# Kernel optimization log

Hardware: AMD Instinct MI355X
Metric: run time of the kernel (lower is better)

## Reference

```python
import jax, jax.numpy as jnp
import numpy as np

D_MODEL = 1024
NUM_HEADS = 16
HEAD_DIM = D_MODEL // NUM_HEADS


def setup_inputs() -> dict:
    key = jax.random.key(0)
    ks = jax.random.split(key, 11)
    B, S = 2, 2048
    sc = 1.0 / np.sqrt(D_MODEL)
    inp = {
        "query": jax.random.normal(ks[0], (B, S, D_MODEL), jnp.float32),
        "key": jax.random.normal(ks[1], (B, S, D_MODEL), jnp.float32),
        "value": jax.random.normal(ks[2], (B, S, D_MODEL), jnp.float32),
        "Wq": jax.random.normal(ks[3], (D_MODEL, D_MODEL), jnp.float32) * sc,
        "bq": jnp.zeros((D_MODEL,), jnp.float32),
        "Wk": jax.random.normal(ks[4], (D_MODEL, D_MODEL), jnp.float32) * sc,
        "bk": jnp.zeros((D_MODEL,), jnp.float32),
        "Wv": jax.random.normal(ks[5], (D_MODEL, D_MODEL), jnp.float32) * sc,
        "bv": jnp.zeros((D_MODEL,), jnp.float32),
        "Wo": jax.random.normal(ks[6], (D_MODEL, D_MODEL), jnp.float32) * sc,
        "bo": jnp.zeros((D_MODEL,), jnp.float32),
    }
    return inp


def _split_heads(x):
    B, S, _ = x.shape
    return x.reshape(B, S, NUM_HEADS, HEAD_DIM).transpose(0, 2, 1, 3)  # [B,H,S,Dh]


def reference(query, key, value, Wq, bq, Wk, bk, Wv, bv, Wo, bo):
    Q = _split_heads(query @ Wq.T + bq)
    K = _split_heads(key @ Wk.T + bk)
    V = _split_heads(value @ Wv.T + bv)
    scores = jnp.einsum("bhqd,bhkd->bhqk", Q, K) / jnp.sqrt(jnp.float32(HEAD_DIM))
    attn = jax.nn.softmax(scores, axis=-1)  # dropout = identity (eval)
    out = jnp.einsum("bhqk,bhkd->bhqd", attn, V)
    B, H, S, Dh = out.shape
    out = out.transpose(0, 2, 1, 3).reshape(B, S, H * Dh)
    return out @ Wo.T + bo
```

## Files before the change

### kernel.cpp

```cpp
#include <hip/hip_runtime.h>
#include <hip/hip_bf16.h>

typedef __attribute__((ext_vector_type(8))) short short8;
typedef __attribute__((ext_vector_type(4))) short short4v;
typedef __attribute__((ext_vector_type(4))) float f32x4;
typedef __attribute__((ext_vector_type(16))) float f32x16;
typedef __attribute__((ext_vector_type(4))) int int4v;
typedef __attribute__((ext_vector_type(2))) int int2v;

#define DEV static __device__ __forceinline__

constexpr int S_LEN   = 2048;
constexpr int DMODEL  = 1024;
constexpr int NHEAD   = 16;
constexpr int DHEAD   = 64;
constexpr int NBATCH  = 2;
constexpr int BHN     = NBATCH * NHEAD;
constexpr int MROWS   = NBATCH * S_LEN;
constexpr int NDIM    = DMODEL;

DEV unsigned short f2b(float f) {
  __hip_bfloat16 h = __float2bfloat16(f);
  return __builtin_bit_cast(unsigned short, h);
}
DEV unsigned pk2(float a, float b) {
  return (unsigned)f2b(a) | ((unsigned)f2b(b) << 16);
}
DEV short8 ld8(const void* p) {
  return *reinterpret_cast<const short8*>(p);
}
DEV f32x4 mfma16(short8 a, short8 b, f32x4 c) {
  return __builtin_amdgcn_mfma_f32_16x16x32_bf16(a, b, c, 0, 0, 0);
}
DEV f32x16 mfma32(short8 a, short8 b, f32x16 c) {
  return __builtin_amdgcn_mfma_f32_32x32x16_bf16(a, b, c, 0, 0, 0);
}
DEV void gload16(const void* g, void* l) {
  __builtin_amdgcn_global_load_lds(
      (const __attribute__((address_space(1))) unsigned*)g,
      (__attribute__((address_space(3))) unsigned*)l, 16, 0, 0);
}

struct CvtArgs {
  const float* src[7];
  unsigned short* dst[7];
  int n4[7];
};

__global__ __launch_bounds__(256) void cvt_bf16(CvtArgs c) {
  const int seg = blockIdx.y;
  const float* __restrict__ s = c.src[seg];
  unsigned short* __restrict__ d = c.dst[seg];
  const int n4 = c.n4[seg];
  for (int i = blockIdx.x * 256 + threadIdx.x; i < n4; i += gridDim.x * 256) {
    f32x4 v = reinterpret_cast<const f32x4*>(s)[i];
    short4v r;
    r[0] = (short)f2b(v[0]); r[1] = (short)f2b(v[1]);
    r[2] = (short)f2b(v[2]); r[3] = (short)f2b(v[3]);
    reinterpret_cast<short4v*>(d)[i] = r;
  }
}

struct GB {
  const unsigned short* A[3];
  const unsigned short* W[3];
  const float* bia[3];
  void* out[3];
  int epi[3];
};

__global__ __launch_bounds__(256, 2) void gemm_bf16(GB g) {
  const int z = blockIdx.z;
  const unsigned short* __restrict__ A = g.A[z];
  const unsigned short* __restrict__ W = g.W[z];
  const float* __restrict__ bia = g.bia[z];
  const int epi = g.epi[z];
  const int bm = blockIdx.y, bn = blockIdx.x;
  const int tid = threadIdx.x, lane = tid & 63, wid = tid >> 6;
  const int wr = wid >> 1, wc = wid & 1;
  const int fr = lane & 15, gq = lane >> 4;

  __shared__ unsigned short As[2][128][32];
  __shared__ unsigned short Bs[2][128][32];

  f32x4 acc[4][4] = {};

  const int srow = lane >> 2;
  const int scol = (lane & 3) * 16;
  const char* aS = (const char*)A + (size_t)(bm * 128 + wid * 16 + srow) * 2048 + scol;
  const char* bS = (const char*)W + (size_t)(bn * 128 + wid * 16 + srow) * 2048 + scol;

  auto stage = [&](int buf, int kt) {
    const int ko = kt * 64;
    char* a0 = (char*)As[buf] + wid * 1024;
    char* b0 = (char*)Bs[buf] + wid * 1024;
    gload16(aS + ko, a0);
    gload16(aS + (size_t)64 * 2048 + ko, a0 + 4096);
    gload16(bS + ko, b0);
    gload16(bS + (size_t)64 * 2048 + ko, b0 + 4096);
  };

  stage(0, 0);
  __syncthreads();
  for (int kt = 0; kt < 32; ++kt) {
    const int buf = kt & 1;
    if (kt + 1 < 32) stage(buf ^ 1, kt + 1);
    short8 af[4], bf4[4];
#pragma unroll
    for (int i = 0; i < 4; ++i) af[i] = ld8(&As[buf][wr * 64 + i * 16 + fr][gq * 8]);
#pragma unroll
    for (int j = 0; j < 4; ++j) bf4[j] = ld8(&Bs[buf][wc * 64 + j * 16 + fr][gq * 8]);
#pragma unroll
    for (int i = 0; i < 4; ++i)
#pragma unroll
      for (int j = 0; j < 4; ++j)
        acc[i][j] = mfma16(af[i], bf4[j], acc[i][j]);
    __syncthreads();
  }

#pragma unroll
  for (int i = 0; i < 4; ++i) {
#pragma unroll
    for (int j = 0; j < 4; ++j) {
#pragma unroll
      for (int r = 0; r < 4; ++r) {
        const int row = bm * 128 + wr * 64 + i * 16 + gq * 4 + r;
        const int col = bn * 128 + wc * 64 + j * 16 + fr;
        float v = acc[i][j][r] + bia[col];
        if (epi == 3) {
          ((float*)g.out[z])[(size_t)row * NDIM + col] = v;
        } else {
          const int b = row >> 11, s = row & (S_LEN - 1);
          const int h = col >> 6,  dh = col & (DHEAD - 1);
          unsigned short* O = (unsigned short*)g.out[z];
          if (epi == 0)      O[((size_t)(b * NHEAD + h) * S_LEN + s) * DHEAD + dh] = f2b(v * 0.125f);
          else if (epi == 1) O[((size_t)(b * NHEAD + h) * S_LEN + s) * DHEAD + dh] = f2b(v);
          else               O[((size_t)(b * NHEAD + h) * DHEAD + dh) * S_LEN + s] = f2b(v);
        }
      }
    }
  }
}

__global__ __launch_bounds__(256, 2) void attn_fwd(
    const unsigned short* __restrict__ Qp,
    const unsigned short* __restrict__ Kp,
    const unsigned short* __restrict__ Vt,
    unsigned short* __restrict__ AO) {
  const int nb = (blockIdx.x & 7) * 64 + (blockIdx.x >> 3);
  const int qt = nb & 15, bh = nb >> 4;
  const int tid = threadIdx.x, lane = tid & 63, wid = tid >> 6;
  const int ql = lane & 31, hi = lane >> 5, l7 = lane & 7, l3 = lane >> 3;

  const unsigned short* Qh = Qp + (size_t)bh * S_LEN * DHEAD;
  const char* Kh = (const char*)(Kp + (size_t)bh * S_LEN * DHEAD);
  const char* Vh = (const char*)(Vt + (size_t)bh * DHEAD * S_LEN);

  __shared__ unsigned short Klds[2][4096];
  __shared__ unsigned short Vlds[2][4096];

  const int q0 = qt * 128 + wid * 32;
  short8 qf[4];
#pragma unroll
  for (int d16 = 0; d16 < 4; ++d16)
    qf[d16] = ld8(Qh + (size_t)(q0 + ql) * DHEAD + d16 * 16 + hi * 8);

  const int swc = (l7 ^ l3) << 4;
  const char* kS = Kh + (wid * 16 + l3) * 128 + swc;
  const char* vS = Vh + (wid * 16 + l3) * 4096 + swc;
  char* kD0 = (char*)Klds[0] + wid * 2048;
  char* vD0 = (char*)Vlds[0] + wid * 2048;
  char* kD1 = (char*)Klds[1] + wid * 2048;
  char* vD1 = (char*)Vlds[1] + wid * 2048;

  int xo[4];
#pragma unroll
  for (int j = 0; j < 4; ++j) xo[j] = ((j * 2 + hi) ^ l7) << 4;

  float m = -1e30f, l = 0.f;
  f32x16 o0 = {}, o1 = {};

  gload16(kS, kD0); gload16(kS + 1024, kD0 + 1024);
  gload16(vS, vD0); gload16(vS + 32768, vD0 + 1024);
  __syncthreads();

  for (int kt = 0; kt < S_LEN / 64; ++kt) {
    const int buf = kt & 1;
    if (kt + 1 < S_LEN / 64) {
      const char* kn = kS + (kt + 1) * 8192;
      const char* vn = vS + (kt + 1) * 128;
      char* kD = buf ? kD0 : kD1;
      char* vD = buf ? vD0 : vD1;
      gload16(kn, kD); gload16(kn + 1024, kD + 1024);
      gload16(vn, vD); gload16(vn + 32768, vD + 1024);
    }
    const char* kb = (const char*)Klds[buf] + ql * 128;
    const char* vb = (const char*)Vlds[buf] + ql * 128;

    f32x16 st0 = {}, st1 = {};
#pragma unroll
    for (int d16 = 0; d16 < 4; ++d16) {
      short8 k0 = ld8(kb + xo[d16]);
      short8 k1 = ld8(kb + 4096 + xo[d16]);
      st0 = mfma32(k0, qf[d16], st0);
      st1 = mfma32(k1, qf[d16], st1);
    }

    float pm = fmaxf(st0[0], st1[0]);
#pragma unroll
    for (int r = 1; r < 16; ++r) pm = fmaxf(pm, fmaxf(st0[r], st1[r]));
    pm = fmaxf(pm, __shfl_xor(pm, 32));

    const float mnew = fmaxf(m, pm);
    const float alpha = __expf(m - mnew);
    m = mnew;
    l *= alpha;
#pragma unroll
    for (int r = 0; r < 16; ++r) { o0[r] *= alpha; o1[r] *= alpha; }

    float tl = 0.f;
#pragma unroll
    for (int r = 0; r < 16; ++r) {
      st0[r] = __expf(st0[r] - mnew); tl += st0[r];
      st1[r] = __expf(st1[r] - mnew); tl += st1[r];
    }
    l += tl + __shfl_xor(tl, 32);

#pragma unroll
    for (int ks = 0; ks < 4; ++ks) {
      const f32x16& p = (ks < 2) ? st0 : st1;
      const int a = 8 * (ks & 1);
      unsigned w0 = pk2(p[a + 0], p[a + 1]);
      unsigned w1 = pk2(p[a + 2], p[a + 3]);
      unsigned w2 = pk2(p[a + 4], p[a + 5]);
      unsigned w3 = pk2(p[a + 6], p[a + 7]);
      unsigned x0 = (unsigned)__shfl_xor((int)w0, 32);
      unsigned x1 = (unsigned)__shfl_xor((int)w1, 32);
      unsigned x2 = (unsigned)__shfl_xor((int)w2, 32);
      unsigned x3 = (unsigned)__shfl_xor((int)w3, 32);
      int4v pi;
      pi[0] = (int)(hi ? x2 : w0);
      pi[1] = (int)(hi ? x3 : w1);
      pi[2] = (int)(hi ? w2 : x0);
      pi[3] = (int)(hi ? w3 : x1);
      short8 pb = __builtin_bit_cast(short8, pi);
      short8 v0 = ld8(vb + xo[ks]);
      short8 v1 = ld8(vb + 4096 + xo[ks]);
      o0 = mfma32(v0, pb, o0);
      o1 = mfma32(v1, pb, o1);
    }
    __syncthreads();
  }

  const float inv = 1.f / l;
  const int b = bh >> 4, h = bh & 15;
  unsigned short* Op = AO + ((size_t)(b * S_LEN + q0 + ql)) * DMODEL + h * DHEAD;
#pragma unroll
  for (int gidx = 0; gidx < 4; ++gidx) {
    int2v s0, s1;
    s0[0] = (int)pk2(o0[gidx * 4 + 0] * inv, o0[gidx * 4 + 1] * inv);
    s0[1] = (int)pk2(o0[gidx * 4 + 2] * inv, o0[gidx * 4 + 3] * inv);
    s1[0] = (int)pk2(o1[gidx * 4 + 0] * inv, o1[gidx * 4 + 1] * inv);
    s1[1] = (int)pk2(o1[gidx * 4 + 2] * inv, o1[gidx * 4 + 3] * inv);
    *reinterpret_cast<int2v*>(Op + 8 * gidx + 4 * hi)      = s0;
    *reinterpret_cast<int2v*>(Op + 32 + 8 * gidx + 4 * hi) = s1;
  }
}

extern "C" void kernel_launch(void* const* d_in, const int* in_sizes, int n_in,
                              void* d_out, int out_size, void* d_ws, size_t ws_size,
                              hipStream_t stream) {
  const float* query = (const float*)d_in[0];
  const float* key   = (const float*)d_in[1];
  const float* value = (const float*)d_in[2];
  const float* Wq = (const float*)d_in[3];  const float* bq = (const float*)d_in[4];
  const float* Wk = (const float*)d_in[5];  const float* bk = (const float*)d_in[6];
  const float* Wv = (const float*)d_in[7];  const float* bv = (const float*)d_in[8];
  const float* Wo = (const float*)d_in[9];  const float* bo = (const float*)d_in[10];

  const size_t MB = 1024u * 1024u;
  unsigned short* Xb  = (unsigned short*)((char*)d_ws + 0 * MB);
  unsigned short* Wb  = (unsigned short*)((char*)d_ws + 24 * MB);
  unsigned short* Wob = (unsigned short*)((char*)d_ws + 30 * MB);
  unsigned short* Qp  = (unsigned short*)((char*)d_ws + 32 * MB);
  unsigned short* Kp  = (unsigned short*)((char*)d_ws + 40 * MB);
  unsigned short* Vt  = (unsigned short*)((char*)d_ws + 48 * MB);
  unsigned short* AOb = (unsigned short*)((char*)d_ws + 0 * MB);

  const int NACT = MROWS * DMODEL;
  const int NWT  = DMODEL * DMODEL;

  CvtArgs ca;
  ca.src[0] = query; ca.dst[0] = Xb;            ca.n4[0] = NACT / 4;
  ca.src[1] = key;   ca.dst[1] = Xb + NACT;     ca.n4[1] = NACT / 4;
  ca.src[2] = value; ca.dst[2] = Xb + 2 * NACT; ca.n4[2] = NACT / 4;
  ca.src[3] = Wq;    ca.dst[3] = Wb;            ca.n4[3] = NWT / 4;
  ca.src[4] = Wk;    ca.dst[4] = Wb + NWT;      ca.n4[4] = NWT / 4;
  ca.src[5] = Wv;    ca.dst[5] = Wb + 2 * NWT;  ca.n4[5] = NWT / 4;
  ca.src[6] = Wo;    ca.dst[6] = Wob;           ca.n4[6] = NWT / 4;
  cvt_bf16<<<dim3(512, 7), 256, 0, stream>>>(ca);

  GB g1;
  g1.A[0] = Xb;            g1.A[1] = Xb + NACT; g1.A[2] = Xb + 2 * NACT;
  g1.W[0] = Wb;            g1.W[1] = Wb + NWT;  g1.W[2] = Wb + 2 * NWT;
  g1.bia[0] = bq;  g1.bia[1] = bk; g1.bia[2] = bv;
  g1.out[0] = Qp;  g1.out[1] = Kp; g1.out[2] = Vt;
  g1.epi[0] = 0;   g1.epi[1] = 1;  g1.epi[2] = 2;
  gemm_bf16<<<dim3(NDIM / 128, MROWS / 128, 3), 256, 0, stream>>>(g1);

  attn_fwd<<<dim3(BHN * 16), 256, 0, stream>>>(Qp, Kp, Vt, AOb);

  GB g2 = {};
  g2.A[0] = AOb; g2.W[0] = Wob; g2.bia[0] = bo; g2.out[0] = d_out; g2.epi[0] = 3;
  gemm_bf16<<<dim3(NDIM / 128, MROWS / 128, 1), 256, 0, stream>>>(g2);
}
```

Before: 164.5 us.

## Split attention KV range across two warp groups and merge partial softmax results

Doubles the attention block to 512 threads, with two groups of four warps each processing half of the key/value sequence in their own double-buffered LDS tiles. The partial (m, l, O) states are merged at the end through LDS, reusing the K/V buffers. It also adds a lazy rescale that only updates the running max when some lane's new max exceeds the old one by more than 8, and reduces the max and sum as trees. The aim is more waves in flight and a shorter serial KV loop per block, at the cost of doubled LDS per block, possible lower blocks per CU, and an extra merge step.

Result: faster. 156.3 us (-5.0%).

```diff
diff --git a/kernel.cpp b/kernel.cpp
--- a/kernel.cpp
+++ b/kernel.cpp
@@ -142,7 +142,7 @@
   }
 }
 
-__global__ __launch_bounds__(256, 2) void attn_fwd(
+__global__ __launch_bounds__(512, 2) void attn_fwd(
     const unsigned short* __restrict__ Qp,
     const unsigned short* __restrict__ Kp,
     const unsigned short* __restrict__ Vt,
@@ -150,28 +150,29 @@
   const int nb = (blockIdx.x & 7) * 64 + (blockIdx.x >> 3);
   const int qt = nb & 15, bh = nb >> 4;
   const int tid = threadIdx.x, lane = tid & 63, wid = tid >> 6;
+  const int qw = wid & 3, hw = wid >> 2;
   const int ql = lane & 31, hi = lane >> 5, l7 = lane & 7, l3 = lane >> 3;
 
   const unsigned short* Qh = Qp + (size_t)bh * S_LEN * DHEAD;
   const char* Kh = (const char*)(Kp + (size_t)bh * S_LEN * DHEAD);
   const char* Vh = (const char*)(Vt + (size_t)bh * DHEAD * S_LEN);
 
-  __shared__ unsigned short Klds[2][4096];
-  __shared__ unsigned short Vlds[2][4096];
-
-  const int q0 = qt * 128 + wid * 32;
+  __shared__ unsigned short Klds[2][2][4096];
+  __shared__ unsigned short Vlds[2][2][4096];
+
+  const int q0 = qt * 128 + qw * 32;
   short8 qf[4];
 #pragma unroll
   for (int d16 = 0; d16 < 4; ++d16)
     qf[d16] = ld8(Qh + (size_t)(q0 + ql) * DHEAD + d16 * 16 + hi * 8);
 
   const int swc = (l7 ^ l3) << 4;
-  const char* kS = Kh + (wid * 16 + l3) * 128 + swc;
-  const char* vS = Vh + (wid * 16 + l3) * 4096 + swc;
-  char* kD0 = (char*)Klds[0] + wid * 2048;
-  char* vD0 = (char*)Vlds[0] + wid * 2048;
-  char* kD1 = (char*)Klds[1] + wid * 2048;
-  char* vD1 = (char*)Vlds[1] + wid * 2048;
+  const char* kS = Kh + (size_t)hw * 16 * 8192 + (qw * 16 + l3) * 128 + swc;
+  const char* vS = Vh + (size_t)hw * 16 * 128 + (qw * 16 + l3) * 4096 + swc;
+  char* kD0 = (char*)Klds[hw][0] + qw * 2048;
+  char* vD0 = (char*)Vlds[hw][0] + qw * 2048;
+  char* kD1 = (char*)Klds[hw][1] + qw * 2048;
+  char* vD1 = (char*)Vlds[hw][1] + qw * 2048;
 
   int xo[4];
 #pragma unroll
@@ -184,9 +185,10 @@
   gload16(vS, vD0); gload16(vS + 32768, vD0 + 1024);
   __syncthreads();
 
-  for (int kt = 0; kt < S_LEN / 64; ++kt) {
+  constexpr int NT = S_LEN / 64 / 2;
+  for (int kt = 0; kt < NT; ++kt) {
     const int buf = kt & 1;
-    if (kt + 1 < S_LEN / 64) {
+    if (kt + 1 < NT) {
       const char* kn = kS + (kt + 1) * 8192;
       const char* vn = vS + (kt + 1) * 128;
       char* kD = buf ? kD0 : kD1;
@@ -194,8 +196,8 @@
       gload16(kn, kD); gload16(kn + 1024, kD + 1024);
       gload16(vn, vD); gload16(vn + 32768, vD + 1024);
     }
-    const char* kb = (const char*)Klds[buf] + ql * 128;
-    const char* vb = (const char*)Vlds[buf] + ql * 128;
+    const char* kb = (const char*)Klds[hw][buf] + ql * 128;
+    const char* vb = (const char*)Vlds[hw][buf] + ql * 128;
 
     f32x16 st0 = {}, st1 = {};
 #pragma unroll
@@ -206,25 +208,39 @@
       st1 = mfma32(k1, qf[d16], st1);
     }
 
-    float pm = fmaxf(st0[0], st1[0]);
-#pragma unroll
-    for (int r = 1; r < 16; ++r) pm = fmaxf(pm, fmaxf(st0[r], st1[r]));
-    pm = fmaxf(pm, __shfl_xor(pm, 32));
-
-    const float mnew = fmaxf(m, pm);
-    const float alpha = __expf(m - mnew);
-    m = mnew;
-    l *= alpha;
-#pragma unroll
-    for (int r = 0; r < 16; ++r) { o0[r] *= alpha; o1[r] *= alpha; }
-
-    float tl = 0.f;
+    float t8[8];
+#pragma unroll
+    for (int r = 0; r < 8; ++r)
+      t8[r] = fmaxf(fmaxf(st0[r], st0[r + 8]), fmaxf(st1[r], st1[r + 8]));
+#pragma unroll
+    for (int s = 4; s; s >>= 1)
+#pragma unroll
+      for (int r = 0; r < s; ++r) t8[r] = fmaxf(t8[r], t8[r + s]);
+    float pm = fmaxf(t8[0], __shfl_xor(t8[0], 32));
+
+    if (!__all(pm <= m + 8.f)) {
+      const float mnew = fmaxf(m, pm);
+      const float alpha = __expf(m - mnew);
+      m = mnew;
+      l *= alpha;
+#pragma unroll
+      for (int r = 0; r < 16; ++r) { o0[r] *= alpha; o1[r] *= alpha; }
+    }
+
 #pragma unroll
     for (int r = 0; r < 16; ++r) {
-      st0[r] = __expf(st0[r] - mnew); tl += st0[r];
-      st1[r] = __expf(st1[r] - mnew); tl += st1[r];
-    }
-    l += tl + __shfl_xor(tl, 32);
+      st0[r] = __expf(st0[r] - m);
+      st1[r] = __expf(st1[r] - m);
+    }
+    float s8[8];
+#pragma unroll
+    for (int r = 0; r < 8; ++r)
+      s8[r] = (st0[r] + st0[r + 8]) + (st1[r] + st1[r + 8]);
+#pragma unroll
+    for (int s = 4; s; s >>= 1)
+#pragma unroll
+      for (int r = 0; r < s; ++r) s8[r] += s8[r + s];
+    l += s8[0] + __shfl_xor(s8[0], 32);
 
 #pragma unroll
     for (int ks = 0; ks < 4; ++ks) {
@@ -252,18 +268,42 @@
     __syncthreads();
   }
 
-  const float inv = 1.f / l;
-  const int b = bh >> 4, h = bh & 15;
-  unsigned short* Op = AO + ((size_t)(b * S_LEN + q0 + ql)) * DMODEL + h * DHEAD;
-#pragma unroll
-  for (int gidx = 0; gidx < 4; ++gidx) {
-    int2v s0, s1;
-    s0[0] = (int)pk2(o0[gidx * 4 + 0] * inv, o0[gidx * 4 + 1] * inv);
-    s0[1] = (int)pk2(o0[gidx * 4 + 2] * inv, o0[gidx * 4 + 3] * inv);
-    s1[0] = (int)pk2(o1[gidx * 4 + 0] * inv, o1[gidx * 4 + 1] * inv);
-    s1[1] = (int)pk2(o1[gidx * 4 + 2] * inv, o1[gidx * 4 + 3] * inv);
-    *reinterpret_cast<int2v*>(Op + 8 * gidx + 4 * hi)      = s0;
-    *reinterpret_cast<int2v*>(Op + 32 + 8 * gidx + 4 * hi) = s1;
+  float* Kf = (float*)&Klds[0][0][0];
+  float* Vf = (float*)&Vlds[0][0][0];
+  if (hw == 1) {
+#pragma unroll
+    for (int r = 0; r < 16; ++r) {
+      Kf[qw * 2048 + r * 64 + lane]        = o0[r];
+      Kf[qw * 2048 + (16 + r) * 64 + lane] = o1[r];
+    }
+    Vf[qw * 128 + lane]      = m;
+    Vf[qw * 128 + 64 + lane] = l;
+  }
+  __syncthreads();
+  if (hw == 0) {
+    const float mb = Vf[qw * 128 + lane];
+    const float lb = Vf[qw * 128 + 64 + lane];
+    const float M  = fmaxf(m, mb);
+    const float wa = __expf(m - M);
+    const float wb = __expf(mb - M);
+    const float inv = 1.f / (wa * l + wb * lb);
+    const int b = bh >> 4, h = bh & 15;
+    unsigned short* Op = AO + ((size_t)(b * S_LEN + q0 + ql)) * DMODEL + h * DHEAD;
+#pragma unroll
+    for (int gidx = 0; gidx < 4; ++gidx) {
+      float f0[4], f1[4];
+#pragma unroll
+      for (int r = 0; r < 4; ++r) {
+        const int rr = gidx * 4 + r;
+        f0[r] = (wa * o0[rr] + wb * Kf[qw * 2048 + rr * 64 + lane]) * inv;
+        f1[r] = (wa * o1[rr] + wb * Kf[qw * 2048 + (16 + rr) * 64 + lane]) * inv;
+      }
+      int2v s0, s1;
+      s0[0] = (int)pk2(f0[0], f0[1]); s0[1] = (int)pk2(f0[2], f0[3]);
+      s1[0] = (int)pk2(f1[0], f1[1]); s1[1] = (int)pk2(f1[2], f1[3]);
+      *reinterpret_cast<int2v*>(Op + 8 * gidx + 4 * hi)      = s0;
+      *reinterpret_cast<int2v*>(Op + 32 + 8 * gidx + 4 * hi) = s1;
+    }
   }
 }
 
@@ -308,7 +348,7 @@
   g1.epi[0] = 0;   g1.epi[1] = 1;  g1.epi[2] = 2;
   gemm_bf16<<<dim3(NDIM / 128, MROWS / 128, 3), 256, 0, stream>>>(g1);
 
-  attn_fwd<<<dim3(BHN * 16), 256, 0, stream>>>(Qp, Kp, Vt, AOb);
+  attn_fwd<<<dim3(BHN * 16), 512, 0, stream>>>(Qp, Kp, Vt, AOb);
 
   GB g2 = {};
   g2.A[0] = AOb; g2.W[0] = Wob; g2.bia[0] = bo; g2.out[0] = d_out; g2.epi[0] = 3;
```
